# Optimization experiments

Hardware: AMD Instinct MI355X
Metric: run time of the kernel (lower is better)

Reference implementation:

```python
import jax, jax.numpy as jnp
import numpy as np

B = 512          # batch size (<= 640 so the original's %640 on row indices is a no-op)
FEATS = 30       # active HalfKP features per position (max pieces minus kings)
NNZ = B * FEATS
FT_OUT = 512
N_FEAT = 40960
N_VFEAT = 640


def setup_inputs() -> dict:
    key = jax.random.key(0)
    ks = jax.random.split(key, 8)
    rows = jnp.repeat(jnp.arange(B, dtype=jnp.int32), FEATS)  # COO batch-row ids
    stm_cols = jax.random.randint(ks[0], (NNZ,), 0, N_FEAT, dtype=jnp.int32)
    nstm_cols = jax.random.randint(ks[1], (NNZ,), 0, N_FEAT, dtype=jnp.int32)
    stm_indices = jnp.stack([rows, stm_cols])    # [2, NNZ]
    nstm_indices = jnp.stack([rows, nstm_cols])  # [2, NNZ]
    values = jnp.ones((NNZ,), jnp.float32)       # NNUE features are 0/1
    s_ft = 1.0 / np.sqrt(N_FEAT)
    s_fft = 1.0 / np.sqrt(N_VFEAT)
    s_out = 1.0 / np.sqrt(2 * FT_OUT)
    return {
        'stm_indices': stm_indices,
        'nstm_indices': nstm_indices,
        'values': values,
        'ft_w': jax.random.normal(ks[2], (FT_OUT, N_FEAT), jnp.float32) * s_ft,
        'ft_b': jax.random.normal(ks[3], (FT_OUT,), jnp.float32) * s_ft,
        'fft_w': jax.random.normal(ks[4], (FT_OUT, N_VFEAT), jnp.float32) * s_fft,
        'fft_b': jax.random.normal(ks[5], (FT_OUT,), jnp.float32) * s_fft,
        'out_w': jax.random.normal(ks[6], (1, 2 * FT_OUT), jnp.float32) * s_out,
        'out_b': jax.random.normal(ks[7], (1,), jnp.float32) * s_out,
    }


def reference(stm_indices, nstm_indices, values, ft_w, ft_b, fft_w, fft_b, out_w, out_b):
    ft_wt = ft_w.T    # [N_FEAT, FT_OUT]
    fft_wt = fft_w.T  # [N_VFEAT, FT_OUT]

    def half_ft(idx):
        # sparse COO (rows, cols) embedding-bag: gather weight columns, scale, segment-sum per row
        rows, cols = idx[0], idx[1]
        g = ft_wt[cols] * values[:, None]            # real HalfKP features
        gv = fft_wt[cols % N_VFEAT] * values[:, None]  # factorized 'virtual' features
        acc = jax.ops.segment_sum(g + gv, rows, num_segments=B)  # [B, FT_OUT]
        return acc + ft_b + fft_b

    stm_ft = half_ft(stm_indices)
    nstm_ft = half_ft(nstm_indices)
    hidden = jnp.clip(jnp.concatenate([stm_ft, nstm_ft], axis=1), 0.0, 1.0)
    return jax.nn.sigmoid(hidden @ out_w.T + out_b)  # [B, 1]
```

## Files before the change

### kernel.cpp

```cpp
#include <hip/hip_runtime.h>
#include <math.h>

#define BATCH   512
#define FEATS   30
#define NNZT    (BATCH * FEATS)
#define FT_OUT  512
#define NFEAT   40960
#define NVFEAT  640

#define FT_TILES  ((FT_OUT / 32) * (NFEAT / 32))
#define FFT_TILES ((FT_OUT / 32) * (NVFEAT / 32))
#define NTILES    (FT_TILES + FFT_TILES)

__device__ inline unsigned int bpack(float a, float b) {
    unsigned int ua = __float_as_uint(a), ub = __float_as_uint(b);
    ua = (ua + 0x7fff + ((ua >> 16) & 1)) >> 16;
    ub = (ub + 0x7fff + ((ub >> 16) & 1)) >> 16;
    return ua | (ub << 16);
}
__device__ inline float bf2f(unsigned short u) {
    return __uint_as_float((unsigned int)u << 16);
}

__global__ __launch_bounds__(256) void transpose_pack(
    const float* __restrict__ ft_w, const float* __restrict__ fft_w,
    unsigned short* __restrict__ ftT, unsigned short* __restrict__ fftT)
{
    __shared__ float tile[4][32][33];
    const int wid  = threadIdx.x >> 6;
    const int lane = threadIdx.x & 63;
    const int t = blockIdx.x * 4 + wid;

    const float* W; unsigned short* T; int C, fb, cb;
    if (t < FT_TILES) {
        W = ft_w;  T = ftT;  C = NFEAT;
        fb = (t & 15) * 32;  cb = (t >> 4) * 32;
    } else {
        int u = t - FT_TILES;
        W = fft_w; T = fftT; C = NVFEAT;
        fb = (u & 15) * 32;  cb = (u >> 4) * 32;
    }

#pragma unroll
    for (int it = 0; it < 4; ++it) {
        const int fi = it * 8 + (lane >> 3);
        const int cq = (lane & 7) * 4;
        const float4 v = *(const float4*)(W + (size_t)(fb + fi) * C + cb + cq);
        tile[wid][cq + 0][fi] = v.x;
        tile[wid][cq + 1][fi] = v.y;
        tile[wid][cq + 2][fi] = v.z;
        tile[wid][cq + 3][fi] = v.w;
    }
    __syncthreads();

#pragma unroll
    for (int it = 0; it < 2; ++it) {
        const int ci = it * 16 + (lane >> 2);
        const int fq = (lane & 3) * 8;
        uint4 o;
        unsigned int* op = (unsigned int*)&o;
#pragma unroll
        for (int j = 0; j < 4; ++j)
            op[j] = bpack(tile[wid][ci][fq + 2 * j],
                          tile[wid][ci][fq + 2 * j + 1]);
        *(uint4*)(T + (size_t)(cb + ci) * FT_OUT + fb + fq) = o;
    }
}

__global__ __launch_bounds__(512) void gather_out(
    const unsigned short* __restrict__ ftT,
    const unsigned short* __restrict__ fftT,
    const int*   __restrict__ stm_idx,
    const int*   __restrict__ nstm_idx,
    const float* __restrict__ values,
    const float* __restrict__ ft_b, const float* __restrict__ fft_b,
    const float* __restrict__ out_w, const float* __restrict__ out_b,
    float*       __restrict__ out)
{
    const int b = blockIdx.x;
    const int f = threadIdx.x;

    __shared__ int   cs[2][FEATS];
    __shared__ float vs[FEATS];
    if (threadIdx.x < FEATS)
        cs[0][threadIdx.x] = stm_idx[NNZT + b * FEATS + threadIdx.x];
    else if (threadIdx.x < 2 * FEATS)
        cs[1][threadIdx.x - FEATS] = nstm_idx[NNZT + b * FEATS + (threadIdx.x - FEATS)];
    else if (threadIdx.x < 3 * FEATS)
        vs[threadIdx.x - 2 * FEATS] = values[b * FEATS + (threadIdx.x - 2 * FEATS)];
    __syncthreads();

    float a0 = 0.0f, a1 = 0.0f;
#pragma unroll
    for (int k = 0; k < FEATS; ++k) {
        const int c0 = cs[0][k];
        const int c1 = cs[1][k];
        const float v = vs[k];
        a0 += (bf2f(ftT[(size_t)c0 * FT_OUT + f]) +
               bf2f(fftT[(size_t)(c0 % NVFEAT) * FT_OUT + f])) * v;
        a1 += (bf2f(ftT[(size_t)c1 * FT_OUT + f]) +
               bf2f(fftT[(size_t)(c1 % NVFEAT) * FT_OUT + f])) * v;
    }

    const float bias = ft_b[f] + fft_b[f];
    const float h0 = fminf(fmaxf(a0 + bias, 0.0f), 1.0f);
    const float h1 = fminf(fmaxf(a1 + bias, 0.0f), 1.0f);

    float total = h0 * out_w[f] + h1 * out_w[FT_OUT + f];
#pragma unroll
    for (int off = 32; off > 0; off >>= 1)
        total += __shfl_down(total, off, 64);

    __shared__ float red[8];
    const int lane = threadIdx.x & 63;
    const int wid  = threadIdx.x >> 6;
    if (lane == 0) red[wid] = total;
    __syncthreads();
    if (threadIdx.x == 0) {
        float s = red[0];
#pragma unroll
        for (int w = 1; w < 8; ++w) s += red[w];
        s += out_b[0];
        out[b] = 1.0f / (1.0f + expf(-s));
    }
}

__global__ __launch_bounds__(512) void halfkp_direct(
    const int* __restrict__ stm_idx, const int* __restrict__ nstm_idx,
    const float* __restrict__ values,
    const float* __restrict__ ft_w, const float* __restrict__ ft_b,
    const float* __restrict__ fft_w, const float* __restrict__ fft_b,
    const float* __restrict__ out_w, const float* __restrict__ out_b,
    float* __restrict__ out)
{
    const int b = blockIdx.x;
    const int f = threadIdx.x;
    const float bias = ft_b[f] + fft_b[f];
    const float* ftrow  = ft_w  + (size_t)f * NFEAT;
    const float* fftrow = fft_w + f * NVFEAT;
    float acc0 = bias, acc1 = bias;
    for (int k = 0; k < FEATS; ++k) {
        int j = b * FEATS + k;
        int c0 = stm_idx[NNZT + j], c1 = nstm_idx[NNZT + j];
        float v = values[j];
        acc0 += (ftrow[c0] + fftrow[c0 % NVFEAT]) * v;
        acc1 += (ftrow[c1] + fftrow[c1 % NVFEAT]) * v;
    }
    const float h0 = fminf(fmaxf(acc0, 0.0f), 1.0f);
    const float h1 = fminf(fmaxf(acc1, 0.0f), 1.0f);
    float total = h0 * out_w[f] + h1 * out_w[FT_OUT + f];
#pragma unroll
    for (int off = 32; off > 0; off >>= 1)
        total += __shfl_down(total, off, 64);
    __shared__ float red[8];
    if ((threadIdx.x & 63) == 0) red[threadIdx.x >> 6] = total;
    __syncthreads();
    if (threadIdx.x == 0) {
        float s = red[0];
#pragma unroll
        for (int w = 1; w < 8; ++w) s += red[w];
        out[b] = 1.0f / (1.0f + expf(-(s + out_b[0])));
    }
}

extern "C" void kernel_launch(void* const* d_in, const int* in_sizes, int n_in,
                              void* d_out, int out_size, void* d_ws, size_t ws_size,
                              hipStream_t stream)
{
    const int*   stm_idx  = (const int*)  d_in[0];
    const int*   nstm_idx = (const int*)  d_in[1];
    const float* values   = (const float*)d_in[2];
    const float* ft_w     = (const float*)d_in[3];
    const float* ft_b     = (const float*)d_in[4];
    const float* fft_w    = (const float*)d_in[5];
    const float* fft_b    = (const float*)d_in[6];
    const float* out_w    = (const float*)d_in[7];
    const float* out_b    = (const float*)d_in[8];
    float*       out      = (float*)d_out;

    const size_t ftT_bytes  = (size_t)NFEAT  * FT_OUT * 2;
    const size_t fftT_bytes = (size_t)NVFEAT * FT_OUT * 2;
    const size_t need = ftT_bytes + fftT_bytes;

    if (ws_size >= need) {
        unsigned short* ftT  = (unsigned short*)d_ws;
        unsigned short* fftT = (unsigned short*)((char*)d_ws + ftT_bytes);

        transpose_pack<<<NTILES / 4, 256, 0, stream>>>(ft_w, fft_w, ftT, fftT);
        gather_out<<<BATCH, 512, 0, stream>>>(ftT, fftT, stm_idx, nstm_idx,
                                              values, ft_b, fft_b, out_w, out_b, out);
    } else {
        halfkp_direct<<<BATCH, 512, 0, stream>>>(stm_idx, nstm_idx, values,
                                                 ft_w, ft_b, fft_w, fft_b,
                                                 out_w, out_b, out);
    }
}
```

Baseline: 157.2 us.

## Split gather work across waves by feature row with 16-byte loads and LDS reduction

The gather kernel now gives each wave a subset of the 120 (half, real/virtual, feature) rows. Each lane loads 8 bf16 values with one 16-byte load and accumulates 8 outputs, replacing per-thread 2-byte loads for every feature. Per-wave partial sums are written to shared memory and reduced across waves before bias, clamp and the output dot product. This widens memory transactions in the gather at the cost of about 32KB of LDS and an extra synchronisation and reduction pass. The transpose-pack kernel, which likely dominates the total time, is unchanged.

```diff
diff --git a/kernel.cpp b/kernel.cpp
--- a/kernel.cpp
+++ b/kernel.cpp
@@ -18,8 +18,11 @@
     ub = (ub + 0x7fff + ((ub >> 16) & 1)) >> 16;
     return ua | (ub << 16);
 }
-__device__ inline float bf2f(unsigned short u) {
-    return __uint_as_float((unsigned int)u << 16);
+__device__ inline float bf2f(unsigned int u) {
+    return __uint_as_float(u << 16);
+}
+__device__ inline float bf2f_hi(unsigned int u) {
+    return __uint_as_float(u & 0xffff0000u);
 }
 
 __global__ __launch_bounds__(256) void transpose_pack(
@@ -77,11 +80,15 @@
     const float* __restrict__ out_w, const float* __restrict__ out_b,
     float*       __restrict__ out)
 {
-    const int b = blockIdx.x;
-    const int f = threadIdx.x;
-
     __shared__ int   cs[2][FEATS];
     __shared__ float vs[FEATS];
+    __shared__ float pacc[8][2][FT_OUT];
+    __shared__ float red[8];
+
+    const int b    = blockIdx.x;
+    const int wid  = threadIdx.x >> 6;
+    const int lane = threadIdx.x & 63;
+
     if (threadIdx.x < FEATS)
         cs[0][threadIdx.x] = stm_idx[NNZT + b * FEATS + threadIdx.x];
     else if (threadIdx.x < 2 * FEATS)
@@ -90,30 +97,50 @@
         vs[threadIdx.x - 2 * FEATS] = values[b * FEATS + (threadIdx.x - 2 * FEATS)];
     __syncthreads();
 
-    float a0 = 0.0f, a1 = 0.0f;
-#pragma unroll
-    for (int k = 0; k < FEATS; ++k) {
-        const int c0 = cs[0][k];
-        const int c1 = cs[1][k];
-        const float v = vs[k];
-        a0 += (bf2f(ftT[(size_t)c0 * FT_OUT + f]) +
-               bf2f(fftT[(size_t)(c0 % NVFEAT) * FT_OUT + f])) * v;
-        a1 += (bf2f(ftT[(size_t)c1 * FT_OUT + f]) +
-               bf2f(fftT[(size_t)(c1 % NVFEAT) * FT_OUT + f])) * v;
-    }
+    const int f0 = lane * 8;
+    float a0[8], a1[8];
+#pragma unroll
+    for (int i = 0; i < 8; ++i) { a0[i] = 0.0f; a1[i] = 0.0f; }
+
+    for (int k = wid; k < 4 * FEATS; k += 8) {
+        const int h = k >= 2 * FEATS;
+        const int j = k - h * 2 * FEATS;
+        const int jj = (j >= FEATS) ? j - FEATS : j;
+        const int c = cs[h][jj];
+        const float v = vs[jj];
+        const unsigned short* rowp = (j >= FEATS)
+            ? fftT + (size_t)(c % NVFEAT) * FT_OUT
+            : ftT  + (size_t)c * FT_OUT;
+        const uint4 r = *(const uint4*)(rowp + f0);
+        const unsigned int* rw = (const unsigned int*)&r;
+        float* acc = h ? a1 : a0;
+#pragma unroll
+        for (int q = 0; q < 4; ++q) {
+            acc[2 * q]     += bf2f(rw[q]) * v;
+            acc[2 * q + 1] += bf2f_hi(rw[q]) * v;
+        }
+    }
+
+#pragma unroll
+    for (int i = 0; i < 8; i += 4) {
+        *(float4*)&pacc[wid][0][f0 + i] = make_float4(a0[i], a0[i+1], a0[i+2], a0[i+3]);
+        *(float4*)&pacc[wid][1][f0 + i] = make_float4(a1[i], a1[i+1], a1[i+2], a1[i+3]);
+    }
+    __syncthreads();
+
+    const int f = threadIdx.x;
+    float s0 = 0.0f, s1 = 0.0f;
+#pragma unroll
+    for (int w = 0; w < 8; ++w) { s0 += pacc[w][0][f]; s1 += pacc[w][1][f]; }
 
     const float bias = ft_b[f] + fft_b[f];
-    const float h0 = fminf(fmaxf(a0 + bias, 0.0f), 1.0f);
-    const float h1 = fminf(fmaxf(a1 + bias, 0.0f), 1.0f);
+    const float h0 = fminf(fmaxf(s0 + bias, 0.0f), 1.0f);
+    const float h1 = fminf(fmaxf(s1 + bias, 0.0f), 1.0f);
 
     float total = h0 * out_w[f] + h1 * out_w[FT_OUT + f];
 #pragma unroll
     for (int off = 32; off > 0; off >>= 1)
         total += __shfl_down(total, off, 64);
-
-    __shared__ float red[8];
-    const int lane = threadIdx.x & 63;
-    const int wid  = threadIdx.x >> 6;
     if (lane == 0) red[wid] = total;
     __syncthreads();
     if (threadIdx.x == 0) {
@@ -180,9 +207,8 @@
 
     const size_t ftT_bytes  = (size_t)NFEAT  * FT_OUT * 2;
     const size_t fftT_bytes = (size_t)NVFEAT * FT_OUT * 2;
-    const size_t need = ftT_bytes + fftT_bytes;
-
-    if (ws_size >= need) {
+
+    if (ws_size >= ftT_bytes + fftT_bytes) {
         unsigned short* ftT  = (unsigned short*)d_ws;
         unsigned short* fftT = (unsigned short*)((char*)d_ws + ftT_bytes);
 
```

Result: no change. 157.6 us (+0.3%).
